# Performance work log

Hardware: AMD Instinct MI355X
Metric: run time of the kernel (lower is better)

## Reference

```python
import jax, jax.numpy as jnp
import numpy as np

HEADS = 8
NQ = 4  # n_qubits


def _apply_rx(state, q, theta):
    # state: (M,2,2,2,2) complex, theta: (M,)
    c = jnp.cos(theta / 2).astype(jnp.complex64)
    s = (-1j * jnp.sin(theta / 2)).astype(jnp.complex64)
    g = jnp.stack([jnp.stack([c, s], -1), jnp.stack([s, c], -1)], -2)  # (M,2,2)
    st = jnp.moveaxis(state, 1 + q, 1)
    st = jnp.einsum('mab,mb...->ma...', g, st)
    return jnp.moveaxis(st, 1, 1 + q)


def _apply_cnot(state, c, t):
    st = jnp.moveaxis(state, [1 + c, 1 + t], [1, 2])  # (M,2(ctrl),2(tgt),...)
    st = jnp.concatenate([st[:, :1], st[:, 1:, ::-1]], axis=1)
    return jnp.moveaxis(st, [1, 2], [1 + c, 1 + t])


def vqc(x, weights):
    # x: (M,4) embedding angles; weights: (L,4) layer RX angles
    M = x.shape[0]
    state = jnp.zeros((M, 2, 2, 2, 2), jnp.complex64).at[:, 0, 0, 0, 0].set(1.0)
    for q in range(NQ):  # AngleEmbedding (RX)
        state = _apply_rx(state, q, x[:, q])
    for l in range(weights.shape[0]):  # BasicEntanglerLayers
        for q in range(NQ):
            state = _apply_rx(state, q, jnp.broadcast_to(weights[l, q], (M,)))
        for q in range(NQ):
            state = _apply_cnot(state, q, (q + 1) % NQ)
    probs = state.real ** 2 + state.imag ** 2  # (M,2,2,2,2)
    z = [jnp.moveaxis(probs, 1 + q, 1)[:, 0].sum((1, 2, 3))
         - jnp.moveaxis(probs, 1 + q, 1)[:, 1].sum((1, 2, 3)) for q in range(NQ)]
    return jnp.stack(z, -1)  # (M,4) PauliZ expvals


def setup_inputs() -> dict:
    key = jax.random.key(0)
    ks = jax.random.split(key, 24)
    B, S, E = 16, 512, 512
    D = E // HEADS
    f = jax.random.normal
    inp = {
        'query': f(ks[0], (B, S, E), jnp.float32),
        'key': f(ks[1], (B, S, E), jnp.float32),
        'value': f(ks[2], (B, S, E), jnp.float32),
        'mask': jnp.ones((B, S, S), jnp.int32),
        'Wq_in': f(ks[3], (NQ, D), jnp.float32) / np.sqrt(D),
        'bq_in': f(ks[4], (NQ,), jnp.float32) / np.sqrt(D),
        'Wk_in': f(ks[5], (NQ, D), jnp.float32) / np.sqrt(D),
        'bk_in': f(ks[6], (NQ,), jnp.float32) / np.sqrt(D),
        'Wv_in': f(ks[7], (NQ, D), jnp.float32) / np.sqrt(D),
        'bv_in': f(ks[8], (NQ,), jnp.float32) / np.sqrt(D),
        'wvq': f(ks[9], (1, NQ), jnp.float32),
        'wvk': f(ks[10], (1, NQ), jnp.float32),
        'wvv': f(ks[11], (1, NQ), jnp.float32),
        'Wq': f(ks[12], (D, NQ), jnp.float32) / np.sqrt(NQ),
        'bq': f(ks[13], (D,), jnp.float32) / np.sqrt(NQ),
        'Wk': f(ks[14], (D, NQ), jnp.float32) / np.sqrt(NQ),
        'bk': f(ks[15], (D,), jnp.float32) / np.sqrt(NQ),
        'Wv': f(ks[16], (D, NQ), jnp.float32) / np.sqrt(NQ),
        'bv': f(ks[17], (D,), jnp.float32) / np.sqrt(NQ),
        'Wo': f(ks[18], (E, 2 * E), jnp.float32) / np.sqrt(2 * E),
        'bo': f(ks[19], (E,), jnp.float32) / np.sqrt(2 * E),
    }
    return inp


def reference(query, key, value, mask, Wq_in, bq_in, Wk_in, bk_in, Wv_in, bv_in,
              wvq, wvk, wvv, Wq, bq, Wk, bk, Wv, bv, Wo, bo):
    B, S, E = query.shape
    H = HEADS
    D = E // H

    def project(x, W_in, b_in, w_vqc, W_out, b_out):
        xh = x.reshape(B, S, H, D)
        xin = jnp.einsum('bshd,qd->bshq', xh, W_in) + b_in  # (B,S,H,NQ)
        xq = vqc(xin.reshape(-1, NQ), w_vqc).reshape(B, S, H, NQ)
        return jnp.einsum('bshq,dq->bshd', xq, W_out) + b_out  # (B,S,H,D)

    Q = project(query, Wq_in, bq_in, wvq, Wq, bq)
    K = project(key, Wk_in, bk_in, wvk, Wk, bk)
    V = project(value, Wv_in, bv_in, wvv, Wv, bv)

    energy = jnp.einsum('bqhd,bkhd->bhqk', Q, K)
    # NOTE: original masked_fill result is discarded (no-op); scale is depth/2
    # due to Python precedence (depth**1/2 == depth/2). Reproduced faithfully.
    attn = jax.nn.softmax(energy / (D / 2.0), axis=-1)
    out = jnp.einsum('bhqv,bvhd->bqhd', attn, V).reshape(B, S, H * D)
    Qf = Q.reshape(B, S, H * D)
    cat = jnp.concatenate([Qf, out], axis=-1)  # (B,S,2E)
    return cat @ Wo.T + bo
```

## Files before the change

### kernel.cpp

```cpp
#include <hip/hip_runtime.h>
#include <hip/hip_bf16.h>

#define B_ 16
#define S_ 512
#define E_ 512
#define H_ 8
#define D_ 64

typedef __hip_bfloat16 bf16;
typedef unsigned short u16;
typedef __attribute__((ext_vector_type(8))) short short8;
typedef __attribute__((ext_vector_type(4))) float floatx4;

__device__ __forceinline__ u16 f2b(float x) {
    bf16 h = __float2bfloat16(x);
    return *reinterpret_cast<u16*>(&h);
}
__device__ __forceinline__ short8 ld8(const u16* p) { return *(const short8*)p; }

template<int CTRL>
__device__ __forceinline__ float qperm(float x) {
    return __builtin_bit_cast(float,
        __builtin_amdgcn_update_dpp(0, __builtin_bit_cast(int, x), CTRL, 0xF, 0xF, true));
}

#define PROJ_ROW_BLOCKS 3072

__global__ __launch_bounds__(256) void proj_kernel(
    const float* __restrict__ q_in, const float* __restrict__ k_in, const float* __restrict__ v_in,
    const float* __restrict__ Wq_in, const float* __restrict__ bq_in,
    const float* __restrict__ Wk_in, const float* __restrict__ bk_in,
    const float* __restrict__ Wv_in, const float* __restrict__ bv_in,
    const float* __restrict__ wvq, const float* __restrict__ wvk, const float* __restrict__ wvv,
    const float* __restrict__ Wq, const float* __restrict__ bq,
    const float* __restrict__ Wk, const float* __restrict__ bk,
    const float* __restrict__ Wv, const float* __restrict__ bv,
    const float* __restrict__ Wo, u16* __restrict__ Wb,
    u16* __restrict__ Qb, u16* __restrict__ Kb, u16* __restrict__ Vb)
{
    if (blockIdx.x >= PROJ_ROW_BLOCKS) {
        const int i = ((blockIdx.x - PROJ_ROW_BLOCKS) * 256 + threadIdx.x) * 8;
        const float4 a = *(const float4*)&Wo[i];
        const float4 b4 = *(const float4*)&Wo[i + 4];
        u16 tmp[8] __attribute__((aligned(16)));
        tmp[0] = f2b(a.x); tmp[1] = f2b(a.y); tmp[2] = f2b(a.z); tmp[3] = f2b(a.w);
        tmp[4] = f2b(b4.x); tmp[5] = f2b(b4.y); tmp[6] = f2b(b4.z); tmp[7] = f2b(b4.w);
        *(short8*)&Wb[i] = *(short8*)tmp;
        return;
    }

    __shared__ __align__(16) float sWin[256];
    __shared__ __align__(16) float sWout[256];
    __shared__ __align__(16) float sbout[64];
    __shared__ float4 sbw;

    const int t = threadIdx.x;
    const int p = blockIdx.x >> 10;

    const float *X, *Win, *bin, *wv, *Wout, *bout;
    u16* dst;
    if (p == 0)      { X = q_in; Win = Wq_in; bin = bq_in; wv = wvq; Wout = Wq; bout = bq; dst = Qb; }
    else if (p == 1) { X = k_in; Win = Wk_in; bin = bk_in; wv = wvk; Wout = Wk; bout = bk; dst = Kb; }
    else             { X = v_in; Win = Wv_in; bin = bv_in; wv = wvv; Wout = Wv; bout = bv; dst = Vb; }

    sWin[t] = Win[t];
    sWout[t] = Wout[t];
    if (t < 64) sbout[t] = bout[t];
    if (t == 0) sbw = make_float4(bin[0] + wv[0], bin[1] + wv[1],
                                  bin[2] + wv[2], bin[3] + wv[3]);
    __syncthreads();

    const int j = t & 3;
    const int m = (blockIdx.x & 1023) * 64 + (t >> 2);
    const int d0 = j * 16;

    const float* xp = X + (size_t)m * 64 + d0;
    float4 xv[4];
#pragma unroll
    for (int i = 0; i < 4; ++i) xv[i] = *(const float4*)(xp + i * 4);

    float part[4] = {0.f, 0.f, 0.f, 0.f};
#pragma unroll
    for (int i = 0; i < 4; ++i) {
#pragma unroll
        for (int q = 0; q < 4; ++q) {
            const float4 w4 = *(const float4*)&sWin[q * 64 + d0 + i * 4];
            part[q] = fmaf(xv[i].x, w4.x, fmaf(xv[i].y, w4.y,
                      fmaf(xv[i].z, w4.z, fmaf(xv[i].w, w4.w, part[q]))));
        }
    }
#pragma unroll
    for (int q = 0; q < 4; ++q) {
        part[q] += qperm<0xB1>(part[q]);
        part[q] += qperm<0x4E>(part[q]);
    }

    const float4 bw = sbw;
    const float c0 = __cosf(part[0] + bw.x);
    const float c1 = __cosf(part[1] + bw.y);
    const float c2 = __cosf(part[2] + bw.z);
    const float c3 = __cosf(part[3] + bw.w);
    const float tt = c2 * c3;
    const float z1 = c0 * c1;
    const float z0 = c1 * tt;
    const float z2 = z1 * c2;
    const float z3 = z1 * tt;

    const int b = m >> 12, s = (m >> 3) & 511, h = m & 7;
    u16* op = dst + ((size_t)(b * 4096 + h * 512 + s)) * 64 + d0;

    u16 tmp[16] __attribute__((aligned(16)));
#pragma unroll
    for (int d = 0; d < 16; ++d) {
        const float4 wo = *(const float4*)&sWout[(d0 + d) * 4];
        const float o = fmaf(z0, wo.x, fmaf(z1, wo.y,
                        fmaf(z2, wo.z, fmaf(z3, wo.w, sbout[d0 + d]))));
        tmp[d] = f2b(o);
    }
    *(short8*)op = *(short8*)tmp;
    *(short8*)(op + 8) = *(short8*)(tmp + 8);
}

__global__ __launch_bounds__(256) void attn_kernel(
    const u16* __restrict__ Qb, const u16* __restrict__ Kb, const u16* __restrict__ Vb,
    u16* __restrict__ Ob)
{
    __shared__ __align__(16) u16 Ks[64][72];
    __shared__ __align__(16) u16 Vt[64][72];
    __shared__ __align__(16) u16 Ps[4][16][72];

    const int t = threadIdx.x, lane = t & 63, w = t >> 6;
    const int bh = blockIdx.x >> 3;
    const int q0 = (blockIdx.x & 7) * 64;
    const int b = bh >> 3, h = bh & 7;

    const u16* Qp = Qb + (size_t)bh * (S_ * D_) + (size_t)q0 * D_;
    const u16* Kp = Kb + (size_t)bh * (S_ * D_);
    const u16* Vp = Vb + (size_t)bh * (S_ * D_);

    const int nl = lane & 15;
    const int kg = (lane >> 4) * 8;

    const short8 qa0 = ld8(&Qp[(w * 16 + nl) * 64 + kg]);
    const short8 qa1 = ld8(&Qp[(w * 16 + nl) * 64 + kg + 32]);

    floatx4 of[4];
    float l_run[4] = {0.f, 0.f, 0.f, 0.f};
#pragma unroll
    for (int nt = 0; nt < 4; ++nt) of[nt] = 0.f;

    const int rK = t & 63, cK = (t >> 6) * 8;
    const int vr0 = (t & 31) * 2, vc = (t >> 5) * 8;

    short8 kA = ld8(&Kp[rK * 64 + cK]);
    short8 kB = ld8(&Kp[rK * 64 + cK + 32]);
    short8 vA = ld8(&Vp[vr0 * 64 + vc]);
    short8 vB = ld8(&Vp[(vr0 + 1) * 64 + vc]);

    for (int ch = 0; ch < 8; ++ch) {
        __syncthreads();
        *(short8*)&Ks[rK][cK] = kA;
        *(short8*)&Ks[rK][cK + 32] = kB;
#pragma unroll
        for (int jj = 0; jj < 8; ++jj) {
            const unsigned pack = (u16)((short*)&vA)[jj] |
                                  ((unsigned)(u16)((short*)&vB)[jj] << 16);
            *(unsigned*)&Vt[vc + jj][vr0] = pack;
        }
        if (ch < 7) {
            const int nb = (ch + 1) * 64;
            kA = ld8(&Kp[(nb + rK) * 64 + cK]);
            kB = ld8(&Kp[(nb + rK) * 64 + cK + 32]);
            vA = ld8(&Vp[(nb + vr0) * 64 + vc]);
            vB = ld8(&Vp[(nb + vr0 + 1) * 64 + vc]);
        }
        __syncthreads();

        floatx4 sf[4];
#pragma unroll
        for (int nt = 0; nt < 4; ++nt) sf[nt] = 0.f;
#pragma unroll
        for (int nt = 0; nt < 4; ++nt) {
            sf[nt] = __builtin_amdgcn_mfma_f32_16x16x32_bf16(qa0, ld8(&Ks[nt * 16 + nl][kg]), sf[nt], 0, 0, 0);
            sf[nt] = __builtin_amdgcn_mfma_f32_16x16x32_bf16(qa1, ld8(&Ks[nt * 16 + nl][kg + 32]), sf[nt], 0, 0, 0);
        }

        const int prow = (lane >> 4) * 4;
#pragma unroll
        for (int nt = 0; nt < 4; ++nt) {
#pragma unroll
            for (int r = 0; r < 4; ++r) {
                const float pv = __expf(sf[nt][r] * 0.03125f);
                l_run[r] += pv;
                Ps[w][prow + r][nt * 16 + nl] = f2b(pv);
            }
        }

        const short8 pa0 = ld8(&Ps[w][nl][kg]);
        const short8 pa1 = ld8(&Ps[w][nl][kg + 32]);
#pragma unroll
        for (int nt = 0; nt < 4; ++nt) {
            of[nt] = __builtin_amdgcn_mfma_f32_16x16x32_bf16(pa0, ld8(&Vt[nt * 16 + nl][kg]), of[nt], 0, 0, 0);
            of[nt] = __builtin_amdgcn_mfma_f32_16x16x32_bf16(pa1, ld8(&Vt[nt * 16 + nl][kg + 32]), of[nt], 0, 0, 0);
        }
    }

    float inv[4];
#pragma unroll
    for (int r = 0; r < 4; ++r) {
        float sum = l_run[r];
#pragma unroll
        for (int off = 1; off < 16; off <<= 1) sum += __shfl_xor(sum, off, 64);
        inv[r] = 1.0f / sum;
    }
    const int srow = q0 + w * 16 + (lane >> 4) * 4;
#pragma unroll
    for (int r = 0; r < 4; ++r) {
        const size_t base = ((size_t)(b * S_ + srow + r)) * E_ + h * 64 + nl;
#pragma unroll
        for (int nt = 0; nt < 4; ++nt)
            Ob[base + nt * 16] = f2b(of[nt][r] * inv[r]);
    }
}

__global__ __launch_bounds__(256) void out_kernel(
    const u16* __restrict__ Qb, const u16* __restrict__ Ob,
    const u16* __restrict__ Wb, const float* __restrict__ bo,
    float* __restrict__ out)
{
    __shared__ __align__(16) u16 As[64][72];
    __shared__ __align__(16) u16 Bs[128][72];

    const int t = threadIdx.x, lane = t & 63, w = t >> 6;
    const int e0 = (blockIdx.x & 3) * 128;
    const int n0 = (blockIdx.x >> 2) * 64;
    const int wr = (w >> 1) * 32, wc = (w & 1) * 64;
    const int nl = lane & 15, kg = (lane >> 4) * 8;

    const int rA = t & 63, cA = (t >> 6) * 8;
    const int rB = t & 127, cB0 = (t >> 7) * 8;
    const u16* wrow = &Wb[(size_t)(e0 + rB) * 1024];

    floatx4 acc[2][4];
#pragma unroll
    for (int i = 0; i < 2; ++i)
#pragma unroll
        for (int jq = 0; jq < 4; ++jq) acc[i][jq] = 0.f;

    auto a_src = [&](int j0, int r, int c) -> const u16* {
        const int n = n0 + r;
        return (j0 < 512)
            ? &Qb[(((size_t)(n >> 9) * 8 + (j0 >> 6)) * 512 + (n & 511)) * 64 + c]
            : &Ob[(size_t)n * 512 + (j0 - 512) + c];
    };

    short8 aA = ld8(a_src(0, rA, cA));
    short8 aB = ld8(a_src(0, rA, cA + 32));
    short8 b0 = ld8(wrow + cB0);
    short8 b1 = ld8(wrow + cB0 + 16);
    short8 b2 = ld8(wrow + cB0 + 32);
    short8 b3 = ld8(wrow + cB0 + 48);

    for (int j0 = 0; j0 < 1024; j0 += 64) {
        __syncthreads();
        *(short8*)&As[rA][cA] = aA;
        *(short8*)&As[rA][cA + 32] = aB;
        *(short8*)&Bs[rB][cB0] = b0;
        *(short8*)&Bs[rB][cB0 + 16] = b1;
        *(short8*)&Bs[rB][cB0 + 32] = b2;
        *(short8*)&Bs[rB][cB0 + 48] = b3;
        if (j0 < 960) {
            const int jn = j0 + 64;
            aA = ld8(a_src(jn, rA, cA));
            aB = ld8(a_src(jn, rA, cA + 32));
            b0 = ld8(wrow + jn + cB0);
            b1 = ld8(wrow + jn + cB0 + 16);
            b2 = ld8(wrow + jn + cB0 + 32);
            b3 = ld8(wrow + jn + cB0 + 48);
        }
        __syncthreads();

        short8 af[2][2], bfr[4][2];
#pragma unroll
        for (int mt = 0; mt < 2; ++mt) {
            af[mt][0] = ld8(&As[wr + mt * 16 + nl][kg]);
            af[mt][1] = ld8(&As[wr + mt * 16 + nl][kg + 32]);
        }
#pragma unroll
        for (int nt = 0; nt < 4; ++nt) {
            bfr[nt][0] = ld8(&Bs[wc + nt * 16 + nl][kg]);
            bfr[nt][1] = ld8(&Bs[wc + nt * 16 + nl][kg + 32]);
        }
#pragma unroll
        for (int mt = 0; mt < 2; ++mt)
#pragma unroll
            for (int nt = 0; nt < 4; ++nt) {
                acc[mt][nt] = __builtin_amdgcn_mfma_f32_16x16x32_bf16(af[mt][0], bfr[nt][0], acc[mt][nt], 0, 0, 0);
                acc[mt][nt] = __builtin_amdgcn_mfma_f32_16x16x32_bf16(af[mt][1], bfr[nt][1], acc[mt][nt], 0, 0, 0);
            }
    }

    const int prow = (lane >> 4) * 4;
#pragma unroll
    for (int mt = 0; mt < 2; ++mt)
#pragma unroll
        for (int r = 0; r < 4; ++r) {
            const int n = n0 + wr + mt * 16 + prow + r;
#pragma unroll
            for (int nt = 0; nt < 4; ++nt) {
                const int e = e0 + wc + nt * 16 + nl;
                out[(size_t)n * 512 + e] = acc[mt][nt][r] + bo[e];
            }
        }
}

extern "C" void kernel_launch(void* const* d_in, const int* in_sizes, int n_in,
                              void* d_out, int out_size, void* d_ws, size_t ws_size,
                              hipStream_t stream)
{
    const float* q_in  = (const float*)d_in[0];
    const float* k_in  = (const float*)d_in[1];
    const float* v_in  = (const float*)d_in[2];
    const float* Wq_in = (const float*)d_in[4];
    const float* bq_in = (const float*)d_in[5];
    const float* Wk_in = (const float*)d_in[6];
    const float* bk_in = (const float*)d_in[7];
    const float* Wv_in = (const float*)d_in[8];
    const float* bv_in = (const float*)d_in[9];
    const float* wvq   = (const float*)d_in[10];
    const float* wvk   = (const float*)d_in[11];
    const float* wvv   = (const float*)d_in[12];
    const float* Wq    = (const float*)d_in[13];
    const float* bq    = (const float*)d_in[14];
    const float* Wk    = (const float*)d_in[15];
    const float* bk    = (const float*)d_in[16];
    const float* Wv    = (const float*)d_in[17];
    const float* bv    = (const float*)d_in[18];
    const float* Wo    = (const float*)d_in[19];
    const float* bo    = (const float*)d_in[20];

    u16* ws = (u16*)d_ws;
    u16* Qb = ws;
    u16* Kb = ws + (size_t)(1 << 22);
    u16* Vb = ws + (size_t)(2 << 22);
    u16* Ob = ws + (size_t)3 * (1 << 22);
    u16* Wb = ws + (size_t)4 * (1 << 22);

    proj_kernel<<<PROJ_ROW_BLOCKS + 256, 256, 0, stream>>>(q_in, k_in, v_in,
        Wq_in, bq_in, Wk_in, bk_in, Wv_in, bv_in,
        wvq, wvk, wvv, Wq, bq, Wk, bk, Wv, bv,
        Wo, Wb, Qb, Kb, Vb);
    attn_kernel<<<1024, 256, 0, stream>>>(Qb, Kb, Vb, Ob);
    out_kernel<<<512, 256, 0, stream>>>(Qb, Ob, Wb, bo, (float*)d_out);
}
```

Before: 190.3 us.

## Double-buffer LDS tiles in attention and output GEMM kernels

Both the attention and the output-projection kernels switch from a single shared-memory tile to two ping-pong buffers. Each iteration now issues the global loads for the next tile, syncs once, computes on the current buffer, then writes the prefetched registers into the other buffer. This removes one __syncthreads per iteration and lets the global-load latency overlap the MFMA work. In exchange, shared memory per block roughly doubles, which may limit how many blocks fit on a CU.

```diff
diff --git a/kernel.cpp b/kernel.cpp
--- a/kernel.cpp
+++ b/kernel.cpp
@@ -125,8 +125,8 @@
     const u16* __restrict__ Qb, const u16* __restrict__ Kb, const u16* __restrict__ Vb,
     u16* __restrict__ Ob)
 {
-    __shared__ __align__(16) u16 Ks[64][72];
-    __shared__ __align__(16) u16 Vt[64][72];
+    __shared__ __align__(16) u16 Ks[2][64][72];
+    __shared__ __align__(16) u16 Vt[2][64][72];
     __shared__ __align__(16) u16 Ps[4][16][72];
 
     const int t = threadIdx.x, lane = t & 63, w = t >> 6;
@@ -152,21 +152,24 @@
     const int rK = t & 63, cK = (t >> 6) * 8;
     const int vr0 = (t & 31) * 2, vc = (t >> 5) * 8;
 
-    short8 kA = ld8(&Kp[rK * 64 + cK]);
-    short8 kB = ld8(&Kp[rK * 64 + cK + 32]);
-    short8 vA = ld8(&Vp[vr0 * 64 + vc]);
-    short8 vB = ld8(&Vp[(vr0 + 1) * 64 + vc]);
-
-    for (int ch = 0; ch < 8; ++ch) {
-        __syncthreads();
-        *(short8*)&Ks[rK][cK] = kA;
-        *(short8*)&Ks[rK][cK + 32] = kB;
+    {
+        short8 kA = ld8(&Kp[rK * 64 + cK]);
+        short8 kB = ld8(&Kp[rK * 64 + cK + 32]);
+        short8 vA = ld8(&Vp[vr0 * 64 + vc]);
+        short8 vB = ld8(&Vp[(vr0 + 1) * 64 + vc]);
+        *(short8*)&Ks[0][rK][cK] = kA;
+        *(short8*)&Ks[0][rK][cK + 32] = kB;
 #pragma unroll
         for (int jj = 0; jj < 8; ++jj) {
             const unsigned pack = (u16)((short*)&vA)[jj] |
                                   ((unsigned)(u16)((short*)&vB)[jj] << 16);
-            *(unsigned*)&Vt[vc + jj][vr0] = pack;
-        }
+            *(unsigned*)&Vt[0][vc + jj][vr0] = pack;
+        }
+    }
+
+    for (int ch = 0; ch < 8; ++ch) {
+        const int cur = ch & 1, nxt = cur ^ 1;
+        short8 kA, kB, vA, vB;
         if (ch < 7) {
             const int nb = (ch + 1) * 64;
             kA = ld8(&Kp[(nb + rK) * 64 + cK]);
@@ -181,8 +184,8 @@
         for (int nt = 0; nt < 4; ++nt) sf[nt] = 0.f;
 #pragma unroll
         for (int nt = 0; nt < 4; ++nt) {
-            sf[nt] = __builtin_amdgcn_mfma_f32_16x16x32_bf16(qa0, ld8(&Ks[nt * 16 + nl][kg]), sf[nt], 0, 0, 0);
-            sf[nt] = __builtin_amdgcn_mfma_f32_16x16x32_bf16(qa1, ld8(&Ks[nt * 16 + nl][kg + 32]), sf[nt], 0, 0, 0);
+            sf[nt] = __builtin_amdgcn_mfma_f32_16x16x32_bf16(qa0, ld8(&Ks[cur][nt * 16 + nl][kg]), sf[nt], 0, 0, 0);
+            sf[nt] = __builtin_amdgcn_mfma_f32_16x16x32_bf16(qa1, ld8(&Ks[cur][nt * 16 + nl][kg + 32]), sf[nt], 0, 0, 0);
         }
 
         const int prow = (lane >> 4) * 4;
@@ -200,8 +203,19 @@
         const short8 pa1 = ld8(&Ps[w][nl][kg + 32]);
 #pragma unroll
         for (int nt = 0; nt < 4; ++nt) {
-            of[nt] = __builtin_amdgcn_mfma_f32_16x16x32_bf16(pa0, ld8(&Vt[nt * 16 + nl][kg]), of[nt], 0, 0, 0);
-            of[nt] = __builtin_amdgcn_mfma_f32_16x16x32_bf16(pa1, ld8(&Vt[nt * 16 + nl][kg + 32]), of[nt], 0, 0, 0);
+            of[nt] = __builtin_amdgcn_mfma_f32_16x16x32_bf16(pa0, ld8(&Vt[cur][nt * 16 + nl][kg]), of[nt], 0, 0, 0);
+            of[nt] = __builtin_amdgcn_mfma_f32_16x16x32_bf16(pa1, ld8(&Vt[cur][nt * 16 + nl][kg + 32]), of[nt], 0, 0, 0);
+        }
+
+        if (ch < 7) {
+            *(short8*)&Ks[nxt][rK][cK] = kA;
+            *(short8*)&Ks[nxt][rK][cK + 32] = kB;
+#pragma unroll
+            for (int jj = 0; jj < 8; ++jj) {
+                const unsigned pack = (u16)((short*)&vA)[jj] |
+                                      ((unsigned)(u16)((short*)&vB)[jj] << 16);
+                *(unsigned*)&Vt[nxt][vc + jj][vr0] = pack;
+            }
         }
     }
 
@@ -228,8 +242,8 @@
     const u16* __restrict__ Wb, const float* __restrict__ bo,
     float* __restrict__ out)
 {
-    __shared__ __align__(16) u16 As[64][72];
-    __shared__ __align__(16) u16 Bs[128][72];
+    __shared__ __align__(16) u16 As[2][64][72];
+    __shared__ __align__(16) u16 Bs[2][128][72];
 
     const int t = threadIdx.x, lane = t & 63, w = t >> 6;
     const int e0 = (blockIdx.x & 3) * 128;
@@ -254,22 +268,26 @@
             : &Ob[(size_t)n * 512 + (j0 - 512) + c];
     };
 
-    short8 aA = ld8(a_src(0, rA, cA));
-    short8 aB = ld8(a_src(0, rA, cA + 32));
-    short8 b0 = ld8(wrow + cB0);
-    short8 b1 = ld8(wrow + cB0 + 16);
-    short8 b2 = ld8(wrow + cB0 + 32);
-    short8 b3 = ld8(wrow + cB0 + 48);
-
-    for (int j0 = 0; j0 < 1024; j0 += 64) {
-        __syncthreads();
-        *(short8*)&As[rA][cA] = aA;
-        *(short8*)&As[rA][cA + 32] = aB;
-        *(short8*)&Bs[rB][cB0] = b0;
-        *(short8*)&Bs[rB][cB0 + 16] = b1;
-        *(short8*)&Bs[rB][cB0 + 32] = b2;
-        *(short8*)&Bs[rB][cB0 + 48] = b3;
-        if (j0 < 960) {
+    {
+        short8 aA = ld8(a_src(0, rA, cA));
+        short8 aB = ld8(a_src(0, rA, cA + 32));
+        short8 b0 = ld8(wrow + cB0);
+        short8 b1 = ld8(wrow + cB0 + 16);
+        short8 b2 = ld8(wrow + cB0 + 32);
+        short8 b3 = ld8(wrow + cB0 + 48);
+        *(short8*)&As[0][rA][cA] = aA;
+        *(short8*)&As[0][rA][cA + 32] = aB;
+        *(short8*)&Bs[0][rB][cB0] = b0;
+        *(short8*)&Bs[0][rB][cB0 + 16] = b1;
+        *(short8*)&Bs[0][rB][cB0 + 32] = b2;
+        *(short8*)&Bs[0][rB][cB0 + 48] = b3;
+    }
+
+    for (int sl = 0; sl < 16; ++sl) {
+        const int cur = sl & 1, nxt = cur ^ 1;
+        const int j0 = sl * 64;
+        short8 aA, aB, b0, b1, b2, b3;
+        if (sl < 15) {
             const int jn = j0 + 64;
             aA = ld8(a_src(jn, rA, cA));
             aB = ld8(a_src(jn, rA, cA + 32));
@@ -283,13 +301,13 @@
         short8 af[2][2], bfr[4][2];
 #pragma unroll
         for (int mt = 0; mt < 2; ++mt) {
-            af[mt][0] = ld8(&As[wr + mt * 16 + nl][kg]);
-            af[mt][1] = ld8(&As[wr + mt * 16 + nl][kg + 32]);
+            af[mt][0] = ld8(&As[cur][wr + mt * 16 + nl][kg]);
+            af[mt][1] = ld8(&As[cur][wr + mt * 16 + nl][kg + 32]);
         }
 #pragma unroll
         for (int nt = 0; nt < 4; ++nt) {
-            bfr[nt][0] = ld8(&Bs[wc + nt * 16 + nl][kg]);
-            bfr[nt][1] = ld8(&Bs[wc + nt * 16 + nl][kg + 32]);
+            bfr[nt][0] = ld8(&Bs[cur][wc + nt * 16 + nl][kg]);
+            bfr[nt][1] = ld8(&Bs[cur][wc + nt * 16 + nl][kg + 32]);
         }
 #pragma unroll
         for (int mt = 0; mt < 2; ++mt)
@@ -298,6 +316,15 @@
                 acc[mt][nt] = __builtin_amdgcn_mfma_f32_16x16x32_bf16(af[mt][0], bfr[nt][0], acc[mt][nt], 0, 0, 0);
                 acc[mt][nt] = __builtin_amdgcn_mfma_f32_16x16x32_bf16(af[mt][1], bfr[nt][1], acc[mt][nt], 0, 0, 0);
             }
+
+        if (sl < 15) {
+            *(short8*)&As[nxt][rA][cA] = aA;
+            *(short8*)&As[nxt][rA][cA + 32] = aB;
+            *(short8*)&Bs[nxt][rB][cB0] = b0;
+            *(short8*)&Bs[nxt][rB][cB0 + 16] = b1;
+            *(short8*)&Bs[nxt][rB][cB0 + 32] = b2;
+            *(short8*)&Bs[nxt][rB][cB0 + 48] = b3;
+        }
     }
 
     const int prow = (lane >> 4) * 4;
```

After: 193.5 us. About the same (+1.7%).

## Process 32 query rows per wave in attention to reuse K/V tiles

Applied to the files above, without the earlier changes.

Each attention block now covers 128 query rows instead of 64, with every wave computing two 16-row M tiles. This reuses each K and V fragment read from LDS across two MFMAs and halves the global K/V loads and LDS staging per query row. The cost is a halved grid (512 blocks), more registers per thread and a larger P buffer in LDS, which may reduce occupancy and latency hiding.

```diff
diff --git a/kernel.cpp b/kernel.cpp
--- a/kernel.cpp
+++ b/kernel.cpp
@@ -127,11 +127,11 @@
 {
     __shared__ __align__(16) u16 Ks[64][72];
     __shared__ __align__(16) u16 Vt[64][72];
-    __shared__ __align__(16) u16 Ps[4][16][72];
+    __shared__ __align__(16) u16 Ps[4][32][72];
 
     const int t = threadIdx.x, lane = t & 63, w = t >> 6;
-    const int bh = blockIdx.x >> 3;
-    const int q0 = (blockIdx.x & 7) * 64;
+    const int bh = blockIdx.x >> 2;
+    const int q0 = (blockIdx.x & 3) * 128;
     const int b = bh >> 3, h = bh & 7;
 
     const u16* Qp = Qb + (size_t)bh * (S_ * D_) + (size_t)q0 * D_;
@@ -141,13 +141,23 @@
     const int nl = lane & 15;
     const int kg = (lane >> 4) * 8;
 
-    const short8 qa0 = ld8(&Qp[(w * 16 + nl) * 64 + kg]);
-    const short8 qa1 = ld8(&Qp[(w * 16 + nl) * 64 + kg + 32]);
-
-    floatx4 of[4];
-    float l_run[4] = {0.f, 0.f, 0.f, 0.f};
-#pragma unroll
-    for (int nt = 0; nt < 4; ++nt) of[nt] = 0.f;
+    short8 qa[2][2];
+#pragma unroll
+    for (int mt = 0; mt < 2; ++mt) {
+        qa[mt][0] = ld8(&Qp[(w * 32 + mt * 16 + nl) * 64 + kg]);
+        qa[mt][1] = ld8(&Qp[(w * 32 + mt * 16 + nl) * 64 + kg + 32]);
+    }
+
+    floatx4 of[2][4];
+    float l_run[2][4];
+#pragma unroll
+    for (int mt = 0; mt < 2; ++mt)
+#pragma unroll
+        for (int r = 0; r < 4; ++r) { l_run[mt][r] = 0.f; }
+#pragma unroll
+    for (int mt = 0; mt < 2; ++mt)
+#pragma unroll
+        for (int nt = 0; nt < 4; ++nt) of[mt][nt] = 0.f;
 
     const int rK = t & 63, cK = (t >> 6) * 8;
     const int vr0 = (t & 31) * 2, vc = (t >> 5) * 8;
@@ -176,50 +186,71 @@
         }
         __syncthreads();
 
-        floatx4 sf[4];
-#pragma unroll
-        for (int nt = 0; nt < 4; ++nt) sf[nt] = 0.f;
+        floatx4 sf[2][4];
+#pragma unroll
+        for (int mt = 0; mt < 2; ++mt)
+#pragma unroll
+            for (int nt = 0; nt < 4; ++nt) sf[mt][nt] = 0.f;
 #pragma unroll
         for (int nt = 0; nt < 4; ++nt) {
-            sf[nt] = __builtin_amdgcn_mfma_f32_16x16x32_bf16(qa0, ld8(&Ks[nt * 16 + nl][kg]), sf[nt], 0, 0, 0);
-            sf[nt] = __builtin_amdgcn_mfma_f32_16x16x32_bf16(qa1, ld8(&Ks[nt * 16 + nl][kg + 32]), sf[nt], 0, 0, 0);
+            const short8 kf0 = ld8(&Ks[nt * 16 + nl][kg]);
+            const short8 kf1 = ld8(&Ks[nt * 16 + nl][kg + 32]);
+#pragma unroll
+            for (int mt = 0; mt < 2; ++mt) {
+                sf[mt][nt] = __builtin_amdgcn_mfma_f32_16x16x32_bf16(qa[mt][0], kf0, sf[mt][nt], 0, 0, 0);
+                sf[mt][nt] = __builtin_amdgcn_mfma_f32_16x16x32_bf16(qa[mt][1], kf1, sf[mt][nt], 0, 0, 0);
+            }
         }
 
         const int prow = (lane >> 4) * 4;
 #pragma unroll
+        for (int mt = 0; mt < 2; ++mt)
+#pragma unroll
+            for (int nt = 0; nt < 4; ++nt) {
+#pragma unroll
+                for (int r = 0; r < 4; ++r) {
+                    const float pv = __expf(sf[mt][nt][r] * 0.03125f);
+                    l_run[mt][r] += pv;
+                    Ps[w][mt * 16 + prow + r][nt * 16 + nl] = f2b(pv);
+                }
+            }
+
+        short8 pa[2][2];
+#pragma unroll
+        for (int mt = 0; mt < 2; ++mt) {
+            pa[mt][0] = ld8(&Ps[w][mt * 16 + nl][kg]);
+            pa[mt][1] = ld8(&Ps[w][mt * 16 + nl][kg + 32]);
+        }
+#pragma unroll
         for (int nt = 0; nt < 4; ++nt) {
-#pragma unroll
-            for (int r = 0; r < 4; ++r) {
-                const float pv = __expf(sf[nt][r] * 0.03125f);
-                l_run[r] += pv;
-                Ps[w][prow + r][nt * 16 + nl] = f2b(pv);
-            }
-        }
-
-        const short8 pa0 = ld8(&Ps[w][nl][kg]);
-        const short8 pa1 = ld8(&Ps[w][nl][kg + 32]);
-#pragma unroll
-        for (int nt = 0; nt < 4; ++nt) {
-            of[nt] = __builtin_amdgcn_mfma_f32_16x16x32_bf16(pa0, ld8(&Vt[nt * 16 + nl][kg]), of[nt], 0, 0, 0);
-            of[nt] = __builtin_amdgcn_mfma_f32_16x16x32_bf16(pa1, ld8(&Vt[nt * 16 + nl][kg + 32]), of[nt], 0, 0, 0);
-        }
-    }
-
-    float inv[4];
-#pragma unroll
-    for (int r = 0; r < 4; ++r) {
-        float sum = l_run[r];
-#pragma unroll
-        for (int off = 1; off < 16; off <<= 1) sum += __shfl_xor(sum, off, 64);
-        inv[r] = 1.0f / sum;
-    }
-    const int srow = q0 + w * 16 + (lane >> 4) * 4;
-#pragma unroll
-    for (int r = 0; r < 4; ++r) {
-        const size_t base = ((size_t)(b * S_ + srow + r)) * E_ + h * 64 + nl;
-#pragma unroll
-        for (int nt = 0; nt < 4; ++nt)
-            Ob[base + nt * 16] = f2b(of[nt][r] * inv[r]);
+            const short8 vf0 = ld8(&Vt[nt * 16 + nl][kg]);
+            const short8 vf1 = ld8(&Vt[nt * 16 + nl][kg + 32]);
+#pragma unroll
+            for (int mt = 0; mt < 2; ++mt) {
+                of[mt][nt] = __builtin_amdgcn_mfma_f32_16x16x32_bf16(pa[mt][0], vf0, of[mt][nt], 0, 0, 0);
+                of[mt][nt] = __builtin_amdgcn_mfma_f32_16x16x32_bf16(pa[mt][1], vf1, of[mt][nt], 0, 0, 0);
+            }
+        }
+    }
+
+#pragma unroll
+    for (int mt = 0; mt < 2; ++mt) {
+        float inv[4];
+#pragma unroll
+        for (int r = 0; r < 4; ++r) {
+            float sum = l_run[mt][r];
+#pragma unroll
+            for (int off = 1; off < 16; off <<= 1) sum += __shfl_xor(sum, off, 64);
+            inv[r] = 1.0f / sum;
+        }
+        const int srow = q0 + w * 32 + mt * 16 + (lane >> 4) * 4;
+#pragma unroll
+        for (int r = 0; r < 4; ++r) {
+            const size_t base = ((size_t)(b * S_ + srow + r)) * E_ + h * 64 + nl;
+#pragma unroll
+            for (int nt = 0; nt < 4; ++nt)
+                Ob[base + nt * 16] = f2b(of[mt][nt][r] * inv[r]);
+        }
     }
 }
 
@@ -350,6 +381,6 @@
         Wq_in, bq_in, Wk_in, bk_in, Wv_in, bv_in,
         wvq, wvk, wvv, Wq, bq, Wk, bk, Wv, bv,
         Wo, Wb, Qb, Kb, Vb);
-    attn_kernel<<<1024, 256, 0, stream>>>(Qb, Kb, Vb, Ob);
+    attn_kernel<<<512, 256, 0, stream>>>(Qb, Kb, Vb, Ob);
     out_kernel<<<512, 256, 0, stream>>>(Qb, Ob, Wb, bo, (float*)d_out);
 }
```

After: 186.0 us. 1.02x faster.
